# Performance work log

Hardware: AMD Instinct MI355X
Metric: run time of the kernel (lower is better)

## Reference

```python
import jax, jax.numpy as jnp
import numpy as np
from jax import lax


def _conv2d(x, w, b):
    # x: [B,C,H,W], w: [O,I,3,3], 'SAME' padding, stride 1
    y = lax.conv_general_dilated(x, w, (1, 1), 'SAME',
                                 dimension_numbers=('NCHW', 'OIHW', 'NCHW'))
    return y + b[None, :, None, None]


def _grid_sample_border(img, grid):
    # img: [B,C,H,W]; grid: [B,H,W,2] with (x,y) in [-1,1]; align_corners=True,
    # bilinear, padding_mode='border' (coords clamped before interpolation).
    B, C, H, W = img.shape
    ix = jnp.clip((grid[..., 0] + 1.0) * (W - 1) / 2.0, 0.0, W - 1.0)
    iy = jnp.clip((grid[..., 1] + 1.0) * (H - 1) / 2.0, 0.0, H - 1.0)
    x0f = jnp.floor(ix)
    y0f = jnp.floor(iy)
    wx = (ix - x0f)[:, None]  # [B,1,H,W]
    wy = (iy - y0f)[:, None]
    x0 = jnp.clip(x0f.astype(jnp.int32), 0, W - 1)
    x1 = jnp.clip(x0 + 1, 0, W - 1)
    y0 = jnp.clip(y0f.astype(jnp.int32), 0, H - 1)
    y1 = jnp.clip(y0 + 1, 0, H - 1)
    flat = img.reshape(B, C, H * W)

    def gather(yi, xi):
        idx = (yi * W + xi).reshape(B, 1, H * W)
        g = jnp.take_along_axis(flat, jnp.broadcast_to(idx, (B, C, H * W)), axis=2)
        return g.reshape(B, C, H, W)

    v00 = gather(y0, x0)
    v01 = gather(y0, x1)
    v10 = gather(y1, x0)
    v11 = gather(y1, x1)
    top = v00 * (1.0 - wx) + v01 * wx
    bot = v10 * (1.0 - wx) + v11 * wx
    return top * (1.0 - wy) + bot * wy


def setup_inputs() -> dict:
    key = jax.random.key(0)
    ks = jax.random.split(key, 4)
    B, C, H, W = 4, 64, 256, 256
    z_real = jax.random.normal(ks[0], (B, C, H, W), dtype=jnp.float32)
    z_imag = jax.random.normal(ks[1], (B, C, H, W), dtype=jnp.float32)
    fan1 = C * 9
    w1 = jax.random.normal(ks[2], (64, C, 3, 3), dtype=jnp.float32) / np.sqrt(fan1)
    b1 = jnp.zeros((64,), dtype=jnp.float32)
    w2 = jax.random.normal(ks[3], (1, 64, 3, 3), dtype=jnp.float32) / np.sqrt(64 * 9)
    b2 = jnp.zeros((1,), dtype=jnp.float32)
    dt = jnp.float32(0.1)
    return {"z_real": z_real, "z_imag": z_imag, "dt": dt,
            "w1": w1, "b1": b1, "w2": w2, "b2": b2}


def reference(z_real, z_imag, dt, w1, b1, w2, b2):
    B, C, H, W = z_real.shape
    # psi_net: conv -> SiLU -> conv, scaled by dt; psi: [B,1,H,W]
    psi = _conv2d(jax.nn.silu(_conv2d(z_real, w1, b1)), w2, b2) * dt
    # curl with replicate padding, central differences
    p = jnp.pad(psi, ((0, 0), (0, 0), (1, 1), (1, 1)), mode='edge')
    u = (p[:, :, 2:, 1:-1] - p[:, :, :-2, 1:-1]) / 2.0
    v = -(p[:, :, 1:-1, 2:] - p[:, :, 1:-1, :-2]) / 2.0
    # normalized flow: [B,H,W,2]
    flow = jnp.concatenate([u / (W / 2.0), v / (H / 2.0)], axis=1).transpose(0, 2, 3, 1)
    yy, xx = jnp.meshgrid(jnp.linspace(-1.0, 1.0, H), jnp.linspace(-1.0, 1.0, W), indexing='ij')
    base = jnp.stack((xx, yy), axis=-1).astype(z_real.dtype)  # [H,W,2]
    sampling_grid = base[None] - flow
    # sample real and imag in one fused gather over 2C channels
    zc = jnp.concatenate([z_real, z_imag], axis=1)  # [B,2C,H,W]
    out = _grid_sample_border(zc, sampling_grid)
    return out  # [B,2C,H,W]: first C channels = real part, last C = imag part
```

## Files before the change

### kernel.cpp

```cpp
#include <hip/hip_runtime.h>
#include <cmath>

namespace {
constexpr int H = 256, W = 256, HWp = H * W;
constexpr size_t PLANE = (size_t)4 * HWp * 64 * 2;
constexpr size_t NEED_FAST = 73728 + 2 * PLANE + (1u << 20);
}

typedef _Float16 f16;
typedef unsigned int u32;
typedef __attribute__((ext_vector_type(4))) _Float16 f16x4;
typedef __attribute__((ext_vector_type(8))) _Float16 f16x8;
typedef __attribute__((ext_vector_type(4))) float f32x4;
typedef __attribute__((ext_vector_type(4))) unsigned int u32x4;

__device__ __forceinline__ void dma16(const char* g, char* l) {
    __builtin_amdgcn_global_load_lds(
        (const __attribute__((address_space(1))) u32*)g,
        (__attribute__((address_space(3))) u32*)l, 16, 0, 0);
}

__global__ void k_wt(const float* __restrict__ w1, f16* __restrict__ w1tb) {
    int i = blockIdx.x * 256 + threadIdx.x;
    if (i >= 64 * 576) return;
    int co = i / 576, r = i - co * 576;
    int ci = r / 9, k9 = r - ci * 9;
    w1tb[(k9 * 64 + co) * 64 + ci] = (f16)w1[i];
}

__global__ __launch_bounds__(256) void k_xt(const float* __restrict__ x,
                                            f16* __restrict__ dst) {
    __shared__ f16 tile[64][80];
    const int t = threadIdx.x;
    const int p0 = blockIdx.x * 64;
    const size_t base = (size_t)blockIdx.y * 64 * HWp;
#pragma unroll
    for (int r = 0; r < 4; ++r) {
        int q = r * 256 + t;
        int ci = q >> 4, px4 = (q & 15) * 4;
        f32x4 v = *reinterpret_cast<const f32x4*>(x + base + (size_t)ci * HWp + p0 + px4);
#pragma unroll
        for (int j = 0; j < 4; ++j) tile[px4 + j][ci] = (f16)v[j];
    }
    __syncthreads();
    const int px = t >> 2, q = t & 3;
    u32x4* d = reinterpret_cast<u32x4*>(dst + ((size_t)blockIdx.y * HWp + p0 + px) * 64 + q * 16);
    const u32x4* s = reinterpret_cast<const u32x4*>(&tile[px][q * 16]);
    d[0] = s[0];
    d[1] = s[1];
}

__global__ __launch_bounds__(256, 2) void k_conv1(
        const f16* __restrict__ Xt,
        const f16* __restrict__ w1tb,
        const float* __restrict__ b1,
        f16* __restrict__ act) {
    __shared__ __align__(16) char lds[43008];
    constexpr int WOFF = 18432;

    const int tid = threadIdx.x;
    const int lane = tid & 63, wid = tid >> 6;
    const int lr = lane & 15, lg = lane >> 4;
    const int wpx = wid & 1, wco = wid >> 1;

    const int bid = blockIdx.x;
    const int swz = (bid & 7) * 256 + (bid >> 3);
    const int b = swz >> 9;
    const int y = (swz >> 1) & 255;
    const int x0 = (swz & 1) << 7;

    const int swzb = (lane ^ ((lane >> 3) & 7)) << 4;

    f32x4 acc[4][2];
#pragma unroll
    for (int m = 0; m < 4; ++m)
#pragma unroll
        for (int n = 0; n < 2; ++n) acc[m][n] = (f32x4)0.f;

    const f16x8 zf = (f16x8)(f16)0.f;

    for (int dyi = 0; dyi < 3; ++dyi) {
        const int yy = y + dyi - 1;
        if ((unsigned)yy >= 256u) continue;

        __syncthreads();
        {
            const char* asrc = (const char*)Xt +
                ((((size_t)b * 256 + yy) * 256 + x0 - 8) * 128) + swzb;
            const char* wsrc = (const char*)w1tb + dyi * 24576 + swzb;
            for (int j = wid; j < 42; j += 4) {
                if (j < 18) dma16(asrc + j * 1024, lds + j * 1024);
                else        dma16(wsrc + (j - 18) * 1024, lds + WOFF + (j - 18) * 1024);
            }
        }
        __syncthreads();

#pragma unroll
        for (int kx = 0; kx < 3; ++kx) {
            const int dx = kx - 1;
            const int gx0 = x0 + wpx * 64 + lr + dx;
            const bool ok0 = (unsigned)gx0 < 256u;
            const bool ok3 = (unsigned)(gx0 + 48) < 256u;
            const int arow = (8 + wpx * 64 + lr + dx) << 7;
            const int axor = (lr + dx) & 7;
#pragma unroll
            for (int c = 0; c < 2; ++c) {
                const int abase = arow + (((c * 4 + lg) ^ axor) << 4);
                f16x8 A0 = *reinterpret_cast<const f16x8*>(lds + abase);
                f16x8 A1 = *reinterpret_cast<const f16x8*>(lds + abase + 2048);
                f16x8 A2 = *reinterpret_cast<const f16x8*>(lds + abase + 4096);
                f16x8 A3 = *reinterpret_cast<const f16x8*>(lds + abase + 6144);
                const int wbase = WOFF + ((kx * 64 + wco * 32 + lr) << 7)
                                + (((c * 4 + lg) ^ (lr & 7)) << 4);
                f16x8 W0 = *reinterpret_cast<const f16x8*>(lds + wbase);
                f16x8 W1 = *reinterpret_cast<const f16x8*>(lds + wbase + 2048);
                A0 = ok0 ? A0 : zf;
                A3 = ok3 ? A3 : zf;
                acc[0][0] = __builtin_amdgcn_mfma_f32_16x16x32_f16(W0, A0, acc[0][0], 0, 0, 0);
                acc[0][1] = __builtin_amdgcn_mfma_f32_16x16x32_f16(W1, A0, acc[0][1], 0, 0, 0);
                acc[1][0] = __builtin_amdgcn_mfma_f32_16x16x32_f16(W0, A1, acc[1][0], 0, 0, 0);
                acc[1][1] = __builtin_amdgcn_mfma_f32_16x16x32_f16(W1, A1, acc[1][1], 0, 0, 0);
                acc[2][0] = __builtin_amdgcn_mfma_f32_16x16x32_f16(W0, A2, acc[2][0], 0, 0, 0);
                acc[2][1] = __builtin_amdgcn_mfma_f32_16x16x32_f16(W1, A2, acc[2][1], 0, 0, 0);
                acc[3][0] = __builtin_amdgcn_mfma_f32_16x16x32_f16(W0, A3, acc[3][0], 0, 0, 0);
                acc[3][1] = __builtin_amdgcn_mfma_f32_16x16x32_f16(W1, A3, acc[3][1], 0, 0, 0);
            }
        }
    }

    float bias[2][4];
#pragma unroll
    for (int n = 0; n < 2; ++n) {
        f32x4 bv = *reinterpret_cast<const f32x4*>(b1 + wco * 32 + n * 16 + lg * 4);
#pragma unroll
        for (int r = 0; r < 4; ++r) bias[n][r] = bv[r];
    }
    const size_t row_base = ((size_t)b * 256 + y) * 256;
#pragma unroll
    for (int m = 0; m < 4; ++m) {
        f16* ap = act + (row_base + x0 + wpx * 64 + m * 16 + lr) * 64 + wco * 32 + lg * 4;
#pragma unroll
        for (int n = 0; n < 2; ++n) {
            f16x4 o;
#pragma unroll
            for (int r = 0; r < 4; ++r) {
                float v = acc[m][n][r] + bias[n][r];
                v = v / (1.f + __expf(-v));
                o[r] = (f16)v;
            }
            *reinterpret_cast<f16x4*>(ap + n * 16) = o;
        }
    }
}

__global__ __launch_bounds__(256) void k_conv2(
        const f16* __restrict__ act, const float* __restrict__ w2,
        const float* __restrict__ b2, const float* __restrict__ dtp,
        float* __restrict__ psi) {
    const int tx = threadIdx.x & 31, ty = threadIdx.x >> 5;
    const int px = blockIdx.x * 32 + tx;
    const int py = blockIdx.y * 8 + ty;
    const int b = blockIdx.z;

    float a0 = 0.f, a1 = 0.f, a2 = 0.f, a3 = 0.f;
#pragma unroll
    for (int dy = -1; dy <= 1; ++dy) {
        const int yy = py + dy;
        if ((unsigned)yy >= (unsigned)H) continue;
#pragma unroll
        for (int dx = -1; dx <= 1; ++dx) {
            const int xx = px + dx;
            const int k9 = (dy + 1) * 3 + (dx + 1);
            if ((unsigned)xx < (unsigned)W) {
                const f16x8* ap = reinterpret_cast<const f16x8*>(
                    act + (((size_t)b * H + yy) * W + xx) * 64);
                const float* wp = w2 + k9;
#pragma unroll
                for (int g = 0; g < 8; ++g) {
                    const f16x8 v = ap[g];
                    const int cb = g * 8;
                    a0 = fmaf((float)v[0], wp[(cb + 0) * 9], a0);
                    a1 = fmaf((float)v[1], wp[(cb + 1) * 9], a1);
                    a2 = fmaf((float)v[2], wp[(cb + 2) * 9], a2);
                    a3 = fmaf((float)v[3], wp[(cb + 3) * 9], a3);
                    a0 = fmaf((float)v[4], wp[(cb + 4) * 9], a0);
                    a1 = fmaf((float)v[5], wp[(cb + 5) * 9], a1);
                    a2 = fmaf((float)v[6], wp[(cb + 6) * 9], a2);
                    a3 = fmaf((float)v[7], wp[(cb + 7) * 9], a3);
                }
            }
        }
    }
    psi[((size_t)b * H + py) * W + px] = ((a0 + a1) + (a2 + a3) + b2[0]) * dtp[0];
}

__global__ __launch_bounds__(256, 4) void k_sample3(
        const f16* __restrict__ Xt_r, const f16* __restrict__ Xt_i,
        const float* __restrict__ psi, float* __restrict__ out) {
    __shared__ int   s_off[4][128];
    __shared__ float s_w[4][128];
    __shared__ __align__(16) float s_stage[64][132];

    const int tid = threadIdx.x;
    const int bid = blockIdx.x;
    const int swz = (bid & 7) * 256 + (bid >> 3);
    const int seg = swz & 1, y = (swz >> 1) & 255, b = swz >> 9;
    const int x0 = seg * 128;

    if (tid < 128) {
        const int px = x0 + tid;
        const float* pb = psi + b * HWp;
        const int yp = min(y + 1, H - 1), ym = max(y - 1, 0);
        const int xp = min(px + 1, W - 1), xm = max(px - 1, 0);
        const float u = 0.5f * (pb[yp * W + px] - pb[ym * W + px]);
        const float v = -0.5f * (pb[y * W + xp] - pb[y * W + xm]);
        const float gx = (-1.f + 2.f * px / (float)(W - 1)) - u * (2.f / (float)W);
        const float gy = (-1.f + 2.f * y / (float)(H - 1)) - v * (2.f / (float)H);
        float ix = fminf(fmaxf((gx + 1.f) * 0.5f * (float)(W - 1), 0.f), (float)(W - 1));
        float iy = fminf(fmaxf((gy + 1.f) * 0.5f * (float)(H - 1), 0.f), (float)(H - 1));
        const float xf = floorf(ix), yf = floorf(iy);
        const float wx = ix - xf, wy = iy - yf;
        const int ix0 = (int)xf, iy0 = (int)yf;
        const int ix1 = min(ix0 + 1, W - 1), iy1 = min(iy0 + 1, H - 1);
        s_off[0][tid] = (iy0 * W + ix0) * 128;
        s_off[1][tid] = (iy0 * W + ix1) * 128;
        s_off[2][tid] = (iy1 * W + ix0) * 128;
        s_off[3][tid] = (iy1 * W + ix1) * 128;
        s_w[0][tid] = (1.f - wx) * (1.f - wy);
        s_w[1][tid] = wx * (1.f - wy);
        s_w[2][tid] = (1.f - wx) * wy;
        s_w[3][tid] = wx * wy;
    }
    __syncthreads();

    const int p = tid >> 1, s = tid & 1;
    const int o0 = s_off[0][p], o1 = s_off[1][p], o2 = s_off[2][p], o3 = s_off[3][p];
    const float w0 = s_w[0][p], w1 = s_w[1][p], w2 = s_w[2][p], w3 = s_w[3][p];
    const int cl = tid >> 5;
    const int pxq = (tid & 31) * 4;
    const size_t obase = (size_t)b * 128 * HWp + (size_t)y * W + x0 + pxq;

#pragma unroll
    for (int pl = 0; pl < 2; ++pl) {
        const char* base = (const char*)(pl ? Xt_i : Xt_r)
                         + (size_t)b * HWp * 128 + s * 64;
        const char* c0 = base + o0;
        const char* c1 = base + o1;
        const char* c2 = base + o2;
        const char* c3 = base + o3;
        f16x8 h00 = *(const f16x8*)(c0);      f16x8 h01 = *(const f16x8*)(c0 + 16);
        f16x8 h02 = *(const f16x8*)(c0 + 32); f16x8 h03 = *(const f16x8*)(c0 + 48);
        f16x8 h10 = *(const f16x8*)(c1);      f16x8 h11 = *(const f16x8*)(c1 + 16);
        f16x8 h12 = *(const f16x8*)(c1 + 32); f16x8 h13 = *(const f16x8*)(c1 + 48);
        f16x8 h20 = *(const f16x8*)(c2);      f16x8 h21 = *(const f16x8*)(c2 + 16);
        f16x8 h22 = *(const f16x8*)(c2 + 32); f16x8 h23 = *(const f16x8*)(c2 + 48);
        f16x8 h30 = *(const f16x8*)(c3);      f16x8 h31 = *(const f16x8*)(c3 + 16);
        f16x8 h32 = *(const f16x8*)(c3 + 32); f16x8 h33 = *(const f16x8*)(c3 + 48);

        const int rb = s << 5;
#pragma unroll
        for (int k = 0; k < 8; ++k) {
            s_stage[rb + k][p] = w0 * (float)h00[k] + w1 * (float)h10[k]
                               + w2 * (float)h20[k] + w3 * (float)h30[k];
            s_stage[rb + 8 + k][p] = w0 * (float)h01[k] + w1 * (float)h11[k]
                                   + w2 * (float)h21[k] + w3 * (float)h31[k];
            s_stage[rb + 16 + k][p] = w0 * (float)h02[k] + w1 * (float)h12[k]
                                    + w2 * (float)h22[k] + w3 * (float)h32[k];
            s_stage[rb + 24 + k][p] = w0 * (float)h03[k] + w1 * (float)h13[k]
                                    + w2 * (float)h23[k] + w3 * (float)h33[k];
        }
        __syncthreads();
#pragma unroll
        for (int k = 0; k < 8; ++k) {
            const int c = cl + (k << 3);
            f32x4 vv = *(const f32x4*)&s_stage[c][pxq];
            *(f32x4*)(out + obase + (size_t)(pl * 64 + c) * HWp) = vv;
        }
        __syncthreads();
    }
}

__global__ __launch_bounds__(256) void k_sample_fb(
        const float* __restrict__ zr, const float* __restrict__ zi,
        const float* __restrict__ psi, float* __restrict__ out) {
    const int tx = threadIdx.x & 31, ty = threadIdx.x >> 5;
    const int px = blockIdx.x * 32 + tx;
    const int py = blockIdx.y * 8 + ty;
    const int b  = blockIdx.z >> 3;
    const int c0 = (blockIdx.z & 7) * 16;

    const float* pb = psi + b * HWp;
    const int yp = min(py + 1, H - 1), ym = max(py - 1, 0);
    const int xp = min(px + 1, W - 1), xm = max(px - 1, 0);
    const float u = 0.5f * (pb[yp * W + px] - pb[ym * W + px]);
    const float v = -0.5f * (pb[py * W + xp] - pb[py * W + xm]);

    const float gx = (-1.f + 2.f * px / (float)(W - 1)) - u * (2.f / (float)W);
    const float gy = (-1.f + 2.f * py / (float)(H - 1)) - v * (2.f / (float)H);

    float ix = fminf(fmaxf((gx + 1.f) * 0.5f * (float)(W - 1), 0.f), (float)(W - 1));
    float iy = fminf(fmaxf((gy + 1.f) * 0.5f * (float)(H - 1), 0.f), (float)(H - 1));
    const float xf = floorf(ix), yf = floorf(iy);
    const float wx = ix - xf, wy = iy - yf;
    const int ix0 = (int)xf, iy0 = (int)yf;
    const int ix1 = min(ix0 + 1, W - 1), iy1 = min(iy0 + 1, H - 1);

    const int o00 = iy0 * W + ix0, o01 = iy0 * W + ix1;
    const int o10 = iy1 * W + ix0, o11 = iy1 * W + ix1;
    const float w00 = (1.f - wx) * (1.f - wy), w01 = wx * (1.f - wy);
    const float w10 = (1.f - wx) * wy, w11 = wx * wy;

    const float* src0 = (c0 < 64) ? (zr + (size_t)b * 64 * HWp + (size_t)c0 * HWp)
                                  : (zi + (size_t)b * 64 * HWp + (size_t)(c0 - 64) * HWp);
    float* ob = out + ((size_t)b * 128 + c0) * HWp + py * W + px;
#pragma unroll
    for (int c = 0; c < 16; ++c) {
        const float* p = src0 + (size_t)c * HWp;
        ob[(size_t)c * HWp] = p[o00] * w00 + p[o01] * w01 + p[o10] * w10 + p[o11] * w11;
    }
}

extern "C" void kernel_launch(void* const* d_in, const int* in_sizes, int n_in,
                              void* d_out, int out_size, void* d_ws, size_t ws_size,
                              hipStream_t stream) {
    const float* z_real = (const float*)d_in[0];
    const float* z_imag = (const float*)d_in[1];
    const float* dt     = (const float*)d_in[2];
    const float* w1     = (const float*)d_in[3];
    const float* b1     = (const float*)d_in[4];
    const float* w2     = (const float*)d_in[5];
    const float* b2     = (const float*)d_in[6];

    float* out = (float*)d_out;
    char* ws = (char*)d_ws;
    f16* w1tb = (f16*)ws;

    hipLaunchKernelGGL(k_wt, dim3(144), dim3(256), 0, stream, w1, w1tb);

    if (ws_size >= NEED_FAST) {
        f16* Xt_r  = (f16*)(ws + 73728);
        f16* Xt_i  = (f16*)(ws + 73728 + PLANE);
        float* psi = (float*)(ws + 73728 + 2 * PLANE);
        f16* act   = (f16*)d_out;

        hipLaunchKernelGGL(k_xt, dim3(HWp / 64, 4), dim3(256), 0, stream, z_real, Xt_r);
        hipLaunchKernelGGL(k_xt, dim3(HWp / 64, 4), dim3(256), 0, stream, z_imag, Xt_i);
        hipLaunchKernelGGL(k_conv1, dim3(2048), dim3(256), 0, stream, Xt_r, w1tb, b1, act);
        hipLaunchKernelGGL(k_conv2, dim3(8, 32, 4), dim3(256), 0, stream, act, w2, b2, dt, psi);
        hipLaunchKernelGGL(k_sample3, dim3(2048), dim3(256), 0, stream,
                           Xt_r, Xt_i, psi, out);
    } else {
        float* psi = (float*)(ws + 73728);
        f16* Xt  = (f16*)((char*)d_out + 4096);
        f16* act = (f16*)((char*)d_out + 4096 + PLANE);

        hipLaunchKernelGGL(k_xt, dim3(HWp / 64, 4), dim3(256), 0, stream, z_real, Xt);
        hipLaunchKernelGGL(k_conv1, dim3(2048), dim3(256), 0, stream, Xt, w1tb, b1, act);
        hipLaunchKernelGGL(k_conv2, dim3(8, 32, 4), dim3(256), 0, stream, act, w2, b2, dt, psi);
        hipLaunchKernelGGL(k_sample_fb, dim3(8, 32, 32), dim3(256), 0, stream,
                           z_real, z_imag, psi, out);
    }
}
```

Measured before the change: 165.0 us.

## Read conv1 weights from global memory and merge transpose launches

conv1 no longer stages weights in LDS. Each lane reads its f16x8 weight fragments directly from global memory (cached in L1/L2), which shrinks LDS per block from 43 KB to 18 KB and raises launch bounds to 3 blocks per SM for more occupancy. The two real/imag transpose launches are also fused into one kernel with a doubled grid. The risk is higher global/L1 load latency in the inner MFMA loop in exchange for fewer LDS copies and better occupancy.

```diff
diff --git a/kernel.cpp b/kernel.cpp
--- a/kernel.cpp
+++ b/kernel.cpp
@@ -28,12 +28,18 @@
     w1tb[(k9 * 64 + co) * 64 + ci] = (f16)w1[i];
 }
 
-__global__ __launch_bounds__(256) void k_xt(const float* __restrict__ x,
-                                            f16* __restrict__ dst) {
+__global__ __launch_bounds__(256) void k_xt2(const float* __restrict__ zr,
+                                             const float* __restrict__ zi,
+                                             f16* __restrict__ Xt_r,
+                                             f16* __restrict__ Xt_i) {
     __shared__ f16 tile[64][80];
     const int t = threadIdx.x;
     const int p0 = blockIdx.x * 64;
-    const size_t base = (size_t)blockIdx.y * 64 * HWp;
+    const int bb = blockIdx.y & 3;
+    const bool im = blockIdx.y >= 4;
+    const float* x = im ? zi : zr;
+    f16* dst = im ? Xt_i : Xt_r;
+    const size_t base = (size_t)bb * 64 * HWp;
 #pragma unroll
     for (int r = 0; r < 4; ++r) {
         int q = r * 256 + t;
@@ -44,19 +50,18 @@
     }
     __syncthreads();
     const int px = t >> 2, q = t & 3;
-    u32x4* d = reinterpret_cast<u32x4*>(dst + ((size_t)blockIdx.y * HWp + p0 + px) * 64 + q * 16);
+    u32x4* d = reinterpret_cast<u32x4*>(dst + ((size_t)bb * HWp + p0 + px) * 64 + q * 16);
     const u32x4* s = reinterpret_cast<const u32x4*>(&tile[px][q * 16]);
     d[0] = s[0];
     d[1] = s[1];
 }
 
-__global__ __launch_bounds__(256, 2) void k_conv1(
+__global__ __launch_bounds__(256, 3) void k_conv1(
         const f16* __restrict__ Xt,
         const f16* __restrict__ w1tb,
         const float* __restrict__ b1,
         f16* __restrict__ act) {
-    __shared__ __align__(16) char lds[43008];
-    constexpr int WOFF = 18432;
+    __shared__ __align__(16) char lds[18432];
 
     const int tid = threadIdx.x;
     const int lane = tid & 63, wid = tid >> 6;
@@ -78,6 +83,7 @@
         for (int n = 0; n < 2; ++n) acc[m][n] = (f32x4)0.f;
 
     const f16x8 zf = (f16x8)(f16)0.f;
+    const f16* Wbase = w1tb + (size_t)(wco * 32 + lr) * 64 + lg * 8;
 
     for (int dyi = 0; dyi < 3; ++dyi) {
         const int yy = y + dyi - 1;
@@ -87,11 +93,8 @@
         {
             const char* asrc = (const char*)Xt +
                 ((((size_t)b * 256 + yy) * 256 + x0 - 8) * 128) + swzb;
-            const char* wsrc = (const char*)w1tb + dyi * 24576 + swzb;
-            for (int j = wid; j < 42; j += 4) {
-                if (j < 18) dma16(asrc + j * 1024, lds + j * 1024);
-                else        dma16(wsrc + (j - 18) * 1024, lds + WOFF + (j - 18) * 1024);
-            }
+            for (int j = wid; j < 18; j += 4)
+                dma16(asrc + j * 1024, lds + j * 1024);
         }
         __syncthreads();
 
@@ -103,6 +106,7 @@
             const bool ok3 = (unsigned)(gx0 + 48) < 256u;
             const int arow = (8 + wpx * 64 + lr + dx) << 7;
             const int axor = (lr + dx) & 7;
+            const f16* Wk = Wbase + (size_t)(dyi * 3 + kx) * 4096;
 #pragma unroll
             for (int c = 0; c < 2; ++c) {
                 const int abase = arow + (((c * 4 + lg) ^ axor) << 4);
@@ -110,10 +114,9 @@
                 f16x8 A1 = *reinterpret_cast<const f16x8*>(lds + abase + 2048);
                 f16x8 A2 = *reinterpret_cast<const f16x8*>(lds + abase + 4096);
                 f16x8 A3 = *reinterpret_cast<const f16x8*>(lds + abase + 6144);
-                const int wbase = WOFF + ((kx * 64 + wco * 32 + lr) << 7)
-                                + (((c * 4 + lg) ^ (lr & 7)) << 4);
-                f16x8 W0 = *reinterpret_cast<const f16x8*>(lds + wbase);
-                f16x8 W1 = *reinterpret_cast<const f16x8*>(lds + wbase + 2048);
+                const f16* Wc = Wk + c * 32;
+                f16x8 W0 = *reinterpret_cast<const f16x8*>(Wc);
+                f16x8 W1 = *reinterpret_cast<const f16x8*>(Wc + 1024);
                 A0 = ok0 ? A0 : zf;
                 A3 = ok3 ? A3 : zf;
                 acc[0][0] = __builtin_amdgcn_mfma_f32_16x16x32_f16(W0, A0, acc[0][0], 0, 0, 0);
@@ -343,8 +346,8 @@
         float* psi = (float*)(ws + 73728 + 2 * PLANE);
         f16* act   = (f16*)d_out;
 
-        hipLaunchKernelGGL(k_xt, dim3(HWp / 64, 4), dim3(256), 0, stream, z_real, Xt_r);
-        hipLaunchKernelGGL(k_xt, dim3(HWp / 64, 4), dim3(256), 0, stream, z_imag, Xt_i);
+        hipLaunchKernelGGL(k_xt2, dim3(HWp / 64, 8), dim3(256), 0, stream,
+                           z_real, z_imag, Xt_r, Xt_i);
         hipLaunchKernelGGL(k_conv1, dim3(2048), dim3(256), 0, stream, Xt_r, w1tb, b1, act);
         hipLaunchKernelGGL(k_conv2, dim3(8, 32, 4), dim3(256), 0, stream, act, w2, b2, dt, psi);
         hipLaunchKernelGGL(k_sample3, dim3(2048), dim3(256), 0, stream,
@@ -354,7 +357,8 @@
         f16* Xt  = (f16*)((char*)d_out + 4096);
         f16* act = (f16*)((char*)d_out + 4096 + PLANE);
 
-        hipLaunchKernelGGL(k_xt, dim3(HWp / 64, 4), dim3(256), 0, stream, z_real, Xt);
+        hipLaunchKernelGGL(k_xt2, dim3(HWp / 64, 4), dim3(256), 0, stream,
+                           z_real, z_real, Xt, Xt);
         hipLaunchKernelGGL(k_conv1, dim3(2048), dim3(256), 0, stream, Xt, w1tb, b1, act);
         hipLaunchKernelGGL(k_conv2, dim3(8, 32, 4), dim3(256), 0, stream, act, w2, b2, dt, psi);
         hipLaunchKernelGGL(k_sample_fb, dim3(8, 32, 32), dim3(256), 0, stream,
```

Result: slower. 171.8 us (+4.1%).
